# Optimization experiments

Hardware: AMD Instinct MI355X
Metric: run time of the kernel (lower is better)

The kernel has to match this reference:

```python
import jax, jax.numpy as jnp
import numpy as np

T, J, IC = 243, 17, 32
C = J * IC            # 544 embed dim
BS = 3                # block_size
NB = T // BS          # 81 num_blocks
K = 6                 # top_k
H = 8                 # num_heads
DEPTH = 2
HID = int(C * 2.0)    # 1088 mlp hidden
EPS = 1e-6


def _ln(x, g, b):
    m = x.mean(-1, keepdims=True)
    v = ((x - m) ** 2).mean(-1, keepdims=True)
    return (x - m) * jax.lax.rsqrt(v + EPS) * g + b


def setup_inputs() -> dict:
    key = jax.random.key(0)
    ks = jax.random.split(key, 16)
    s = 0.02
    B = 512
    return {
        "x": jax.random.normal(ks[0], (B, T, J, IC), jnp.float32),
        "pos_embed": s * jax.random.normal(ks[1], (1, T, C), jnp.float32),
        "fc1_w": s * jax.random.normal(ks[2], (NB, NB), jnp.float32),
        "fc2_w": s * jax.random.normal(ks[3], (NB, NB), jnp.float32),
        "ln1_g": jnp.ones((DEPTH, C), jnp.float32),
        "ln1_b": jnp.zeros((DEPTH, C), jnp.float32),
        "qkv_w": s * jax.random.normal(ks[4], (DEPTH, 3 * C, C), jnp.float32),
        "qkv_b": jnp.zeros((DEPTH, 3 * C), jnp.float32),
        "proj_w": s * jax.random.normal(ks[5], (DEPTH, C, C), jnp.float32),
        "proj_b": jnp.zeros((DEPTH, C), jnp.float32),
        "ln2_g": jnp.ones((DEPTH, C), jnp.float32),
        "ln2_b": jnp.zeros((DEPTH, C), jnp.float32),
        "mfc1_w": s * jax.random.normal(ks[6], (DEPTH, HID, C), jnp.float32),
        "mfc1_b": jnp.zeros((DEPTH, HID), jnp.float32),
        "mfc2_w": s * jax.random.normal(ks[7], (DEPTH, C, HID), jnp.float32),
        "mfc2_b": jnp.zeros((DEPTH, C), jnp.float32),
        "lnf_g": jnp.ones((C,), jnp.float32),
        "lnf_b": jnp.zeros((C,), jnp.float32),
        "wm2_w": s * jax.random.normal(ks[8], (K,), jnp.float32),
        "wm2_b": jnp.zeros((1,), jnp.float32),
    }


def reference(x, pos_embed, fc1_w, fc2_w, ln1_g, ln1_b, qkv_w, qkv_b,
              proj_w, proj_b, ln2_g, ln2_b, mfc1_w, mfc1_b, mfc2_w, mfc2_b,
              lnf_g, lnf_b, wm2_w, wm2_b):
    B = x.shape[0]
    x = x.reshape(B, T, C) + pos_embed                       # [B,T,C]
    # time_shift: zero-pad one frame at the front, keep first T rows, first C/2 chans
    shifted = jnp.pad(x, ((0, 0), (1, 0), (0, 0)))[:, :T, :C // 2]
    x = jnp.concatenate([shifted, x[:, :, C // 2:]], axis=2)
    # block pooling
    xb = x.reshape(B, NB, BS, C).mean(axis=2)                # [B,NB,C]
    # BlockAttention: global avg over C -> gated MLP -> topk -> gather
    y = xb.mean(axis=2)                                      # [B,NB]
    y = jax.nn.sigmoid(jnp.maximum(y @ fc1_w.T, 0.0) @ fc2_w.T)
    _, idx = jax.lax.top_k(y, K)                             # [B,K]
    t = jnp.take_along_axis(xb, idx[:, :, None], axis=1)     # [B,K,C]
    scale = (C // H) ** -0.5
    for i in range(DEPTH):
        h = _ln(t, ln1_g[i], ln1_b[i])
        qkv = (h @ qkv_w[i].T + qkv_b[i]).reshape(B, K, 3, H, C // H)
        q, k, v = qkv[:, :, 0], qkv[:, :, 1], qkv[:, :, 2]   # [B,K,H,hd]
        attn = jax.nn.softmax(jnp.einsum('bnhd,bmhd->bhnm', q, k) * scale, axis=-1)
        o = jnp.einsum('bhnm,bmhd->bnhd', attn, v).reshape(B, K, C)
        t = t + o @ proj_w[i].T + proj_b[i]
        h = _ln(t, ln2_g[i], ln2_b[i])
        h = jax.nn.gelu(h @ mfc1_w[i].T + mfc1_b[i], approximate=False)
        t = t + (h @ mfc2_w[i].T + mfc2_b[i])
    t = _ln(t, lnf_g, lnf_b)
    out = jnp.einsum('bkc,k->bc', t, wm2_w) + wm2_b          # Conv1d(K,1,ks=1)
    return out.reshape(B, 1, J, C // J)
```

## Files before the change

### kernel.cpp

```cpp
#include <hip/hip_runtime.h>
#include <hip/hip_bf16.h>
#include <math.h>

#define TT 243
#define CC 544
#define NBB 81
#define KK 6
#define HH 8
#define HD 68
#define DEPTH 2
#define HID 1088
#define BB 512
#define MTOK 3072
#define EPSF 1e-6f

typedef __attribute__((ext_vector_type(8))) short bf16x8;
typedef __attribute__((ext_vector_type(4))) float f32x4;

__device__ __forceinline__ __hip_bfloat16 f2b(float f) { return __float2bfloat16(f); }
__device__ __forceinline__ unsigned short f2bu(float f) {
    __hip_bfloat16 h = __float2bfloat16(f);
    return *(unsigned short*)&h;
}
__device__ __forceinline__ float b2f_lo(unsigned int u) { return __uint_as_float(u << 16); }
__device__ __forceinline__ float b2f_hi(unsigned int u) { return __uint_as_float(u & 0xffff0000u); }

#define E0 443904
#define E1 591872
#define E2 887808
#define E3 1183744

#define RS_BLOCKS 3888
#define PS_BLOCKS 8
#define WC_BLOCKS 4624
#define BW_GRID (RS_BLOCKS + PS_BLOCKS + WC_BLOCKS)

__global__ __launch_bounds__(256, 4) void bw_kernel(
    const float* __restrict__ x,
    const float* __restrict__ pos,
    const float* __restrict__ qkvw, const float* __restrict__ projw,
    const float* __restrict__ mfc1w, const float* __restrict__ mfc2w,
    unsigned short* __restrict__ wbf,
    float* __restrict__ L,
    float* __restrict__ R,
    float* __restrict__ pLR)
{
    const int blk = blockIdx.x;
    const int tid = threadIdx.x;

    if (blk < RS_BLOCKS) {
        const int w = tid >> 6;
        const int lane = tid & 63;
        const int oct = lane & 7;
        const int rsub = lane >> 3;
        const int r = (blk * 4 + w) * 8 + rsub;
        const float4* xr = (const float4*)x + (size_t)r * 136;
        float4 xs[17];
#pragma unroll
        for (int j = 0; j < 17; ++j) xs[j] = xr[oct + j * 8];
        float aL = 0.0f, aR = 0.0f;
#pragma unroll
        for (int j = 0; j < 17; ++j) {
            const float s = (xs[j].x + xs[j].y) + (xs[j].z + xs[j].w);
            if (j < 8) aL += s;
            else if (j == 8) { if (oct < 4) aL += s; else aR += s; }
            else aR += s;
        }
#pragma unroll
        for (int m = 1; m < 8; m <<= 1) {
            aL += __shfl_xor(aL, m);
            aR += __shfl_xor(aR, m);
        }
        if (oct == 0) { L[r] = aL; R[r] = aR; }
        return;
    }

    if (blk < RS_BLOCKS + PS_BLOCKS) {
        const int w = tid >> 6;
        const int lane = tid & 63;
        const int oct = lane & 7;
        const int rsub = lane >> 3;
        const int r = (blk - RS_BLOCKS) * 32 + w * 8 + rsub;
        const int rc = (r < TT) ? r : (TT - 1);
        const float4* pr = (const float4*)pos + (size_t)rc * 136;
        float4 xs[17];
#pragma unroll
        for (int j = 0; j < 17; ++j) xs[j] = pr[oct + j * 8];
        float aL = 0.0f, aR = 0.0f;
#pragma unroll
        for (int j = 0; j < 17; ++j) {
            const float s = (xs[j].x + xs[j].y) + (xs[j].z + xs[j].w);
            if (j < 8) aL += s;
            else if (j == 8) { if (oct < 4) aL += s; else aR += s; }
            else aR += s;
        }
#pragma unroll
        for (int m = 1; m < 8; m <<= 1) {
            aL += __shfl_xor(aL, m);
            aR += __shfl_xor(aR, m);
        }
        if (oct == 0 && r < TT) { pLR[r] = aL; pLR[TT + r] = aR; }
        return;
    }

    const int i = (blk - RS_BLOCKS - PS_BLOCKS) * 256 + tid;
    if (i < E3) {
        float4 v;
        if (i < E0)      v = ((const float4*)qkvw)[i];
        else if (i < E1) v = ((const float4*)projw)[i - E0];
        else if (i < E2) v = ((const float4*)mfc1w)[i - E1];
        else             v = ((const float4*)mfc2w)[i - E2];
        ushort4 o;
        o.x = f2bu(v.x); o.y = f2bu(v.y); o.z = f2bu(v.z); o.w = f2bu(v.w);
        ((ushort4*)wbf)[i] = o;
    }
}

__global__ __launch_bounds__(128) void select_kernel(
    const float* __restrict__ L,
    const float* __restrict__ R,
    const float* __restrict__ pLR,
    const float* __restrict__ fc1,
    const float* __restrict__ fc2,
    const float* __restrict__ x,
    const float* __restrict__ pos,
    const float* __restrict__ ln1g,
    const float* __restrict__ ln1b,
    float* __restrict__ t,
    unsigned short* __restrict__ hb)
{
    const int b = blockIdx.x;
    const int tid = threadIdx.x;
    __shared__ float sy[NBB], sz[NBB], swv[NBB];
    __shared__ int sidx[KK];
    __shared__ __align__(16) float st[KK][CC];

    const int w = tid >> 6;
    const int lane = tid & 63;
    const float4* x4 = (const float4*)x;
    const float4* p4 = (const float4*)pos;

    if (tid < NBB) {
        const int n = tid;
        const float* Lb = L + (size_t)b * TT;
        const float* Rb = R + (size_t)b * TT;
        const float* pL = pLR;
        const float* pR = pLR + TT;
        float s = Lb[3 * n] + Lb[3 * n + 1] + Rb[3 * n] + Rb[3 * n + 1] + Rb[3 * n + 2]
                + pL[3 * n] + pL[3 * n + 1] + pR[3 * n] + pR[3 * n + 1] + pR[3 * n + 2];
        if (n > 0) s += Lb[3 * n - 1] + pL[3 * n - 1];
        sy[n] = s * (1.0f / (3.0f * (float)CC));
    }
    __syncthreads();
    if (tid < NBB) {
        float s = 0.0f;
        for (int j = 0; j < NBB; ++j) s += fc1[tid * NBB + j] * sy[j];
        sz[tid] = fmaxf(s, 0.0f);
    }
    __syncthreads();
    if (tid < NBB) {
        float s = 0.0f;
        for (int j = 0; j < NBB; ++j) s += fc2[tid * NBB + j] * sz[j];
        swv[tid] = 1.0f / (1.0f + expf(-s));
    }
    __syncthreads();
    if (w == 0) {
        float va = (lane < NBB) ? swv[lane] : -1e30f;
        float vb = (lane + 64 < NBB) ? swv[lane + 64] : -1e30f;
        const int ia = lane, ib = lane + 64;
        for (int kk = 0; kk < KK; ++kk) {
            float v = va; int idx = ia;
            if (vb > v) { v = vb; idx = ib; }
#pragma unroll
            for (int m = 1; m < 64; m <<= 1) {
                const float ov = __shfl_xor(v, m);
                const int oi = __shfl_xor(idx, m);
                if (ov > v || (ov == v && oi < idx)) { v = ov; idx = oi; }
            }
            if (lane == 0) sidx[kk] = idx;
            if (ia == idx) va = -1e30f;
            if (ib == idx) vb = -1e30f;
        }
    }
    __syncthreads();

    for (int i = tid; i < KK * 136; i += 128) {
        const int k = i / 136;
        const int c4 = i - k * 136;
        const int n = sidx[k];
        const int shift = (c4 < 68) ? -1 : 0;
        float ax = 0.f, ay = 0.f, az = 0.f, aw = 0.f;
#pragma unroll
        for (int i2 = 0; i2 < 3; ++i2) {
            const int ttr = 3 * n + i2 + shift;
            if (ttr >= 0) {
                const float4 xv = x4[((size_t)b * TT + ttr) * 136 + c4];
                const float4 pv = p4[(size_t)ttr * 136 + c4];
                ax += xv.x + pv.x; ay += xv.y + pv.y; az += xv.z + pv.z; aw += xv.w + pv.w;
            }
        }
        const float inv3 = 1.0f / 3.0f;
        const float4 a = make_float4(ax * inv3, ay * inv3, az * inv3, aw * inv3);
        *(float4*)&st[k][c4 * 4] = a;
        ((float4*)t)[((size_t)b * KK + k) * 136 + c4] = a;
    }
    __syncthreads();

    for (int k = w; k < KK; k += 2) {
        float s = 0.0f, s2 = 0.0f;
        for (int c = lane; c < CC; c += 64) { const float v = st[k][c]; s += v; s2 += v * v; }
#pragma unroll
        for (int off = 32; off; off >>= 1) {
            s += __shfl_xor(s, off);
            s2 += __shfl_xor(s2, off);
        }
        const float m = s / (float)CC;
        const float inv = rsqrtf(s2 / (float)CC - m * m + EPSF);
        for (int c4 = lane; c4 < 136; c4 += 64) {
            const float4 v = *(const float4*)&st[k][c4 * 4];
            const float4 gv = ((const float4*)ln1g)[c4];
            const float4 bv = ((const float4*)ln1b)[c4];
            ushort4 o;
            o.x = f2bu((v.x - m) * inv * gv.x + bv.x);
            o.y = f2bu((v.y - m) * inv * gv.y + bv.y);
            o.z = f2bu((v.z - m) * inv * gv.z + bv.z);
            o.w = f2bu((v.w - m) * inv * gv.w + bv.w);
            ((ushort4*)hb)[((size_t)b * KK + k) * 136 + c4] = o;
        }
    }
}

__global__ __launch_bounds__(256) void ln_bf16_kernel(
    const float* __restrict__ X,
    const float* __restrict__ g,
    const float* __restrict__ bta,
    unsigned short* __restrict__ Y)
{
    const int row = blockIdx.x * 4 + (threadIdx.x >> 6);
    const int lane = threadIdx.x & 63;
    const float4* xr4 = (const float4*)(X + (size_t)row * CC);
    const float4 v0 = xr4[lane];
    const float4 v1 = xr4[lane + 64];
    float4 v2 = make_float4(0.f, 0.f, 0.f, 0.f);
    if (lane < 8) v2 = xr4[lane + 128];
    float s = (v0.x + v0.y + v0.z + v0.w) + (v1.x + v1.y + v1.z + v1.w)
            + (v2.x + v2.y + v2.z + v2.w);
    float s2 = (v0.x * v0.x + v0.y * v0.y + v0.z * v0.z + v0.w * v0.w)
             + (v1.x * v1.x + v1.y * v1.y + v1.z * v1.z + v1.w * v1.w)
             + (v2.x * v2.x + v2.y * v2.y + v2.z * v2.z + v2.w * v2.w);
#pragma unroll
    for (int off = 32; off; off >>= 1) {
        s += __shfl_xor(s, off);
        s2 += __shfl_xor(s2, off);
    }
    const float m = s / (float)CC;
    const float inv = rsqrtf(s2 / (float)CC - m * m + EPSF);
    ushort4* yr = (ushort4*)(Y + (size_t)row * CC);
    {
        const float4 gv = ((const float4*)g)[lane];
        const float4 bv = ((const float4*)bta)[lane];
        ushort4 o;
        o.x = f2bu((v0.x - m) * inv * gv.x + bv.x);
        o.y = f2bu((v0.y - m) * inv * gv.y + bv.y);
        o.z = f2bu((v0.z - m) * inv * gv.z + bv.z);
        o.w = f2bu((v0.w - m) * inv * gv.w + bv.w);
        yr[lane] = o;
    }
    {
        const float4 gv = ((const float4*)g)[lane + 64];
        const float4 bv = ((const float4*)bta)[lane + 64];
        ushort4 o;
        o.x = f2bu((v1.x - m) * inv * gv.x + bv.x);
        o.y = f2bu((v1.y - m) * inv * gv.y + bv.y);
        o.z = f2bu((v1.z - m) * inv * gv.z + bv.z);
        o.w = f2bu((v1.w - m) * inv * gv.w + bv.w);
        yr[lane + 64] = o;
    }
    if (lane < 8) {
        const float4 gv = ((const float4*)g)[lane + 128];
        const float4 bv = ((const float4*)bta)[lane + 128];
        ushort4 o;
        o.x = f2bu((v2.x - m) * inv * gv.x + bv.x);
        o.y = f2bu((v2.y - m) * inv * gv.y + bv.y);
        o.z = f2bu((v2.z - m) * inv * gv.z + bv.z);
        o.w = f2bu((v2.w - m) * inv * gv.w + bv.w);
        yr[lane + 128] = o;
    }
}

template <int ACT, int RES, int OBF>
__global__ __launch_bounds__(256) void gemm_mfma_kernel(
    const unsigned short* __restrict__ X,
    const unsigned short* __restrict__ W,
    const float* __restrict__ bias,
    const float* __restrict__ R,
    void* __restrict__ Y,
    int M, int N, int Kd)
{
    const int bm = blockIdx.y * 128;
    const int bn = blockIdx.x * 128;
    const int tid = threadIdx.x;
    const int K8 = Kd >> 3;

    __shared__ __align__(16) short As[128][40];
    __shared__ __align__(16) short Bs[128][40];

    const int r0 = tid >> 2;
    const int c0 = tid & 3;
    const int r1 = r0 + 64;

    const uint4* Xu = (const uint4*)X;
    const uint4* Wu = (const uint4*)W;

    const int wid = tid >> 6;
    const int lane = tid & 63;
    const int wm = (wid >> 1) * 64;
    const int wn = (wid & 1) * 64;
    const int l16 = lane & 15;
    const int l4 = lane >> 4;
    const int koff = l4 * 8;

    f32x4 acc[4][4] = {};

    const int wr0 = min(bn + r0, N - 1);
    const int wr1 = min(bn + r1, N - 1);

    uint4 a0 = Xu[(size_t)(bm + r0) * K8 + c0];
    uint4 a1 = Xu[(size_t)(bm + r1) * K8 + c0];
    uint4 b0 = Wu[(size_t)wr0 * K8 + c0];
    uint4 b1 = Wu[(size_t)wr1 * K8 + c0];

    const int nk = Kd >> 5;
    for (int kt = 0; kt < nk; ++kt) {
        __syncthreads();
        *(uint4*)&As[r0][c0 * 8] = a0;
        *(uint4*)&As[r1][c0 * 8] = a1;
        *(uint4*)&Bs[r0][c0 * 8] = b0;
        *(uint4*)&Bs[r1][c0 * 8] = b1;
        __syncthreads();

        const bool more = (kt + 1 < nk);
        uint4 na0, na1, nb0, nb1;
        if (more) {
            const int kc = (kt + 1) * 4 + c0;
            na0 = Xu[(size_t)(bm + r0) * K8 + kc];
            na1 = Xu[(size_t)(bm + r1) * K8 + kc];
            nb0 = Wu[(size_t)wr0 * K8 + kc];
            nb1 = Wu[(size_t)wr1 * K8 + kc];
        }

        bf16x8 af[4], bf[4];
#pragma unroll
        for (int mf = 0; mf < 4; ++mf) af[mf] = *(const bf16x8*)&As[wm + mf * 16 + l16][koff];
#pragma unroll
        for (int nf = 0; nf < 4; ++nf) bf[nf] = *(const bf16x8*)&Bs[wn + nf * 16 + l16][koff];
#pragma unroll
        for (int mf = 0; mf < 4; ++mf)
#pragma unroll
            for (int nf = 0; nf < 4; ++nf)
                acc[mf][nf] = __builtin_amdgcn_mfma_f32_16x16x32_bf16(af[mf], bf[nf], acc[mf][nf], 0, 0, 0);

        if (more) { a0 = na0; a1 = na1; b0 = nb0; b1 = nb1; }
    }

#pragma unroll
    for (int nf = 0; nf < 4; ++nf) {
        const int col = bn + wn + nf * 16 + l16;
        if (col < N) {
            const float bs = bias[col];
#pragma unroll
            for (int mf = 0; mf < 4; ++mf) {
#pragma unroll
                for (int j = 0; j < 4; ++j) {
                    const int row = bm + wm + mf * 16 + l4 * 4 + j;
                    float v = acc[mf][nf][j] + bs;
                    if (ACT == 1) v = 0.5f * v * (1.0f + erff(v * 0.70710678118654752f));
                    if (RES) v += R[(size_t)row * N + col];
                    if (OBF) ((__hip_bfloat16*)Y)[(size_t)row * N + col] = f2b(v);
                    else     ((float*)Y)[(size_t)row * N + col] = v;
                }
            }
        }
    }
}

__global__ __launch_bounds__(512) void attn_kernel(
    const unsigned short* __restrict__ qkv,
    __hip_bfloat16* __restrict__ o)
{
    const int b = blockIdx.x;
    __shared__ __align__(16) float sq[KK * 3 * CC];
    __shared__ float sp[HH][40];
    const int tid = threadIdx.x;

    const uint4* src4 = (const uint4*)(qkv + (size_t)b * KK * 3 * CC);
    for (int i = tid; i < (KK * 3 * CC) / 8; i += 512) {
        const uint4 u = src4[i];
        float4 f0, f1;
        f0.x = b2f_lo(u.x); f0.y = b2f_hi(u.x);
        f0.z = b2f_lo(u.y); f0.w = b2f_hi(u.y);
        f1.x = b2f_lo(u.z); f1.y = b2f_hi(u.z);
        f1.z = b2f_lo(u.w); f1.w = b2f_hi(u.w);
        ((float4*)sq)[2 * i] = f0;
        ((float4*)sq)[2 * i + 1] = f1;
    }
    __syncthreads();

    const int h = tid >> 6;
    const int lane = tid & 63;
    const float scl = rsqrtf((float)HD);

    if (lane < KK * KK) {
        const int n = lane / KK, m = lane - (lane / KK) * KK;
        const float* qp = &sq[n * (3 * CC) + 0 * CC + h * HD];
        const float* kp = &sq[m * (3 * CC) + 1 * CC + h * HD];
        float s = 0.0f;
#pragma unroll 4
        for (int d = 0; d < HD; ++d) s += qp[d] * kp[d];
        sp[h][lane] = s * scl;
    }
    __syncthreads();
    if (lane < KK) {
        const int n = lane;
        float mx = -1e30f;
#pragma unroll
        for (int m = 0; m < KK; ++m) mx = fmaxf(mx, sp[h][n * KK + m]);
        float e[KK];
        float sum = 0.0f;
#pragma unroll
        for (int m = 0; m < KK; ++m) { e[m] = expf(sp[h][n * KK + m] - mx); sum += e[m]; }
        const float inv = 1.0f / sum;
#pragma unroll
        for (int m = 0; m < KK; ++m) sp[h][n * KK + m] = e[m] * inv;
    }
    __syncthreads();
    for (int i = tid; i < KK * CC; i += 512) {
        const int n = i / CC;
        const int cd = i - n * CC;
        const int hh = cd / HD;
        const int d = cd - hh * HD;
        float acc = 0.0f;
#pragma unroll
        for (int m = 0; m < KK; ++m)
            acc += sp[hh][n * KK + m] * sq[m * (3 * CC) + 2 * CC + hh * HD + d];
        o[(size_t)b * KK * CC + i] = f2b(acc);
    }
}

__global__ __launch_bounds__(256) void final_kernel(
    const float* __restrict__ t,
    const float* __restrict__ g,
    const float* __restrict__ bta,
    const float* __restrict__ wm2w,
    const float* __restrict__ wm2b,
    float* __restrict__ out)
{
    const int b = blockIdx.x;
    const int tid = threadIdx.x;
    __shared__ float st[KK][CC];
    __shared__ float sm[KK], si[KK];
    const float* tb = t + (size_t)b * KK * CC;
    for (int i = tid; i < KK * CC; i += 256) st[i / CC][i % CC] = tb[i];
    __syncthreads();
    const int wid = tid >> 6, lane = tid & 63;
    for (int r = wid; r < KK; r += 4) {
        float s = 0.0f, s2 = 0.0f;
        for (int c = lane; c < CC; c += 64) { const float v = st[r][c]; s += v; s2 += v * v; }
#pragma unroll
        for (int off = 32; off; off >>= 1) { s += __shfl_xor(s, off); s2 += __shfl_xor(s2, off); }
        if (lane == 0) {
            const float m = s / (float)CC;
            sm[r] = m;
            si[r] = rsqrtf(s2 / (float)CC - m * m + EPSF);
        }
    }
    __syncthreads();
    const float w0 = wm2w[0], w1 = wm2w[1], w2 = wm2w[2], w3 = wm2w[3], w4 = wm2w[4], w5 = wm2w[5];
    const float wb = wm2b[0];
    for (int c = tid; c < CC; c += 256) {
        const float gg = g[c], bb = bta[c];
        float acc = wb;
        acc += w0 * ((st[0][c] - sm[0]) * si[0] * gg + bb);
        acc += w1 * ((st[1][c] - sm[1]) * si[1] * gg + bb);
        acc += w2 * ((st[2][c] - sm[2]) * si[2] * gg + bb);
        acc += w3 * ((st[3][c] - sm[3]) * si[3] * gg + bb);
        acc += w4 * ((st[4][c] - sm[4]) * si[4] * gg + bb);
        acc += w5 * ((st[5][c] - sm[5]) * si[5] * gg + bb);
        out[(size_t)b * CC + c] = acc;
    }
}

extern "C" void kernel_launch(void* const* d_in, const int* in_sizes, int n_in,
                              void* d_out, int out_size, void* d_ws, size_t ws_size,
                              hipStream_t stream)
{
    const float* x      = (const float*)d_in[0];
    const float* pos    = (const float*)d_in[1];
    const float* fc1_w  = (const float*)d_in[2];
    const float* fc2_w  = (const float*)d_in[3];
    const float* ln1_g  = (const float*)d_in[4];
    const float* ln1_b  = (const float*)d_in[5];
    const float* qkv_w  = (const float*)d_in[6];
    const float* qkv_b  = (const float*)d_in[7];
    const float* proj_w = (const float*)d_in[8];
    const float* proj_b = (const float*)d_in[9];
    const float* ln2_g  = (const float*)d_in[10];
    const float* ln2_b  = (const float*)d_in[11];
    const float* mfc1_w = (const float*)d_in[12];
    const float* mfc1_b = (const float*)d_in[13];
    const float* mfc2_w = (const float*)d_in[14];
    const float* mfc2_b = (const float*)d_in[15];
    const float* lnf_g  = (const float*)d_in[16];
    const float* lnf_b  = (const float*)d_in[17];
    const float* wm2_w  = (const float*)d_in[18];
    const float* wm2_b  = (const float*)d_in[19];

    float* ws = (float*)d_ws;
    float* L    = ws;
    float* R    = L + 124416;
    float* pLR  = R + 124416;
    float* t    = pLR + 512;
    unsigned short* qkvb = (unsigned short*)(t + (size_t)MTOK * CC);
    unsigned short* hb  = qkvb + (size_t)MTOK * 3 * CC;
    unsigned short* ob  = hb + (size_t)MTOK * CC;
    unsigned short* gb  = ob + (size_t)MTOK * CC;
    unsigned short* wbf = gb + (size_t)MTOK * HID;

    unsigned short* wqkv = wbf;
    unsigned short* wprj = wbf + 1775616;
    unsigned short* wf1  = wbf + 2367488;
    unsigned short* wf2  = wbf + 3551232;

    bw_kernel<<<BW_GRID, 256, 0, stream>>>(
        x, pos, qkv_w, proj_w, mfc1_w, mfc2_w, wbf, L, R, pLR);

    select_kernel<<<BB, 128, 0, stream>>>(
        L, R, pLR, fc1_w, fc2_w, x, pos, ln1_g, ln1_b, t, hb);

    for (int i = 0; i < DEPTH; ++i) {
        if (i > 0) {
            ln_bf16_kernel<<<MTOK / 4, 256, 0, stream>>>(t, ln1_g + i * CC, ln1_b + i * CC, hb);
        }
        gemm_mfma_kernel<0, 0, 1><<<dim3(13, 24), 256, 0, stream>>>(
            hb, wqkv + (size_t)i * 1632 * 544, qkv_b + (size_t)i * 3 * CC,
            nullptr, qkvb, MTOK, 3 * CC, CC);
        attn_kernel<<<BB, 512, 0, stream>>>(qkvb, (__hip_bfloat16*)ob);
        gemm_mfma_kernel<0, 1, 0><<<dim3(5, 24), 256, 0, stream>>>(
            ob, wprj + (size_t)i * 544 * 544, proj_b + (size_t)i * CC,
            t, t, MTOK, CC, CC);
        ln_bf16_kernel<<<MTOK / 4, 256, 0, stream>>>(t, ln2_g + i * CC, ln2_b + i * CC, hb);
        gemm_mfma_kernel<1, 0, 1><<<dim3(9, 24), 256, 0, stream>>>(
            hb, wf1 + (size_t)i * HID * 544, mfc1_b + (size_t)i * HID,
            nullptr, gb, MTOK, HID, CC);
        gemm_mfma_kernel<0, 1, 0><<<dim3(5, 24), 256, 0, stream>>>(
            gb, wf2 + (size_t)i * 544 * HID, mfc2_b + (size_t)i * CC,
            t, t, MTOK, CC, HID);
    }

    final_kernel<<<BB, 256, 0, stream>>>(t, lnf_g, lnf_b, wm2_w, wm2_b, (float*)d_out);
}
```

Measured before the change: 272.7 us.

## Fuse LayerNorm into GEMM A-tile loading and drop standalone LN kernels

```diff
diff --git a/kernel.cpp b/kernel.cpp
--- a/kernel.cpp
+++ b/kernel.cpp
@@ -124,21 +124,24 @@
     const float* __restrict__ fc2,
     const float* __restrict__ x,
     const float* __restrict__ pos,
-    const float* __restrict__ ln1g,
-    const float* __restrict__ ln1b,
-    float* __restrict__ t,
-    unsigned short* __restrict__ hb)
+    float* __restrict__ t)
 {
     const int b = blockIdx.x;
     const int tid = threadIdx.x;
+    __shared__ float sf1[NBB * NBB];
+    __shared__ float sf2[NBB * NBB];
     __shared__ float sy[NBB], sz[NBB], swv[NBB];
     __shared__ int sidx[KK];
-    __shared__ __align__(16) float st[KK][CC];
 
     const int w = tid >> 6;
     const int lane = tid & 63;
     const float4* x4 = (const float4*)x;
     const float4* p4 = (const float4*)pos;
+
+    for (int i = tid; i < NBB * NBB; i += 128) {
+        sf1[i] = fc1[i];
+        sf2[i] = fc2[i];
+    }
 
     if (tid < NBB) {
         const int n = tid;
@@ -154,13 +157,13 @@
     __syncthreads();
     if (tid < NBB) {
         float s = 0.0f;
-        for (int j = 0; j < NBB; ++j) s += fc1[tid * NBB + j] * sy[j];
+        for (int j = 0; j < NBB; ++j) s += sf1[tid * NBB + j] * sy[j];
         sz[tid] = fmaxf(s, 0.0f);
     }
     __syncthreads();
     if (tid < NBB) {
         float s = 0.0f;
-        for (int j = 0; j < NBB; ++j) s += fc2[tid * NBB + j] * sz[j];
+        for (int j = 0; j < NBB; ++j) s += sf2[tid * NBB + j] * sz[j];
         swv[tid] = 1.0f / (1.0f + expf(-s));
     }
     __syncthreads();
@@ -200,100 +203,19 @@
             }
         }
         const float inv3 = 1.0f / 3.0f;
-        const float4 a = make_float4(ax * inv3, ay * inv3, az * inv3, aw * inv3);
-        *(float4*)&st[k][c4 * 4] = a;
-        ((float4*)t)[((size_t)b * KK + k) * 136 + c4] = a;
-    }
-    __syncthreads();
-
-    for (int k = w; k < KK; k += 2) {
-        float s = 0.0f, s2 = 0.0f;
-        for (int c = lane; c < CC; c += 64) { const float v = st[k][c]; s += v; s2 += v * v; }
-#pragma unroll
-        for (int off = 32; off; off >>= 1) {
-            s += __shfl_xor(s, off);
-            s2 += __shfl_xor(s2, off);
-        }
-        const float m = s / (float)CC;
-        const float inv = rsqrtf(s2 / (float)CC - m * m + EPSF);
-        for (int c4 = lane; c4 < 136; c4 += 64) {
-            const float4 v = *(const float4*)&st[k][c4 * 4];
-            const float4 gv = ((const float4*)ln1g)[c4];
-            const float4 bv = ((const float4*)ln1b)[c4];
-            ushort4 o;
-            o.x = f2bu((v.x - m) * inv * gv.x + bv.x);
-            o.y = f2bu((v.y - m) * inv * gv.y + bv.y);
-            o.z = f2bu((v.z - m) * inv * gv.z + bv.z);
-            o.w = f2bu((v.w - m) * inv * gv.w + bv.w);
-            ((ushort4*)hb)[((size_t)b * KK + k) * 136 + c4] = o;
-        }
-    }
-}
-
-__global__ __launch_bounds__(256) void ln_bf16_kernel(
-    const float* __restrict__ X,
-    const float* __restrict__ g,
-    const float* __restrict__ bta,
-    unsigned short* __restrict__ Y)
-{
-    const int row = blockIdx.x * 4 + (threadIdx.x >> 6);
-    const int lane = threadIdx.x & 63;
-    const float4* xr4 = (const float4*)(X + (size_t)row * CC);
-    const float4 v0 = xr4[lane];
-    const float4 v1 = xr4[lane + 64];
-    float4 v2 = make_float4(0.f, 0.f, 0.f, 0.f);
-    if (lane < 8) v2 = xr4[lane + 128];
-    float s = (v0.x + v0.y + v0.z + v0.w) + (v1.x + v1.y + v1.z + v1.w)
-            + (v2.x + v2.y + v2.z + v2.w);
-    float s2 = (v0.x * v0.x + v0.y * v0.y + v0.z * v0.z + v0.w * v0.w)
-             + (v1.x * v1.x + v1.y * v1.y + v1.z * v1.z + v1.w * v1.w)
-             + (v2.x * v2.x + v2.y * v2.y + v2.z * v2.z + v2.w * v2.w);
-#pragma unroll
-    for (int off = 32; off; off >>= 1) {
-        s += __shfl_xor(s, off);
-        s2 += __shfl_xor(s2, off);
-    }
-    const float m = s / (float)CC;
-    const float inv = rsqrtf(s2 / (float)CC - m * m + EPSF);
-    ushort4* yr = (ushort4*)(Y + (size_t)row * CC);
-    {
-        const float4 gv = ((const float4*)g)[lane];
-        const float4 bv = ((const float4*)bta)[lane];
-        ushort4 o;
-        o.x = f2bu((v0.x - m) * inv * gv.x + bv.x);
-        o.y = f2bu((v0.y - m) * inv * gv.y + bv.y);
-        o.z = f2bu((v0.z - m) * inv * gv.z + bv.z);
-        o.w = f2bu((v0.w - m) * inv * gv.w + bv.w);
-        yr[lane] = o;
-    }
-    {
-        const float4 gv = ((const float4*)g)[lane + 64];
-        const float4 bv = ((const float4*)bta)[lane + 64];
-        ushort4 o;
-        o.x = f2bu((v1.x - m) * inv * gv.x + bv.x);
-        o.y = f2bu((v1.y - m) * inv * gv.y + bv.y);
-        o.z = f2bu((v1.z - m) * inv * gv.z + bv.z);
-        o.w = f2bu((v1.w - m) * inv * gv.w + bv.w);
-        yr[lane + 64] = o;
-    }
-    if (lane < 8) {
-        const float4 gv = ((const float4*)g)[lane + 128];
-        const float4 bv = ((const float4*)bta)[lane + 128];
-        ushort4 o;
-        o.x = f2bu((v2.x - m) * inv * gv.x + bv.x);
-        o.y = f2bu((v2.y - m) * inv * gv.y + bv.y);
-        o.z = f2bu((v2.z - m) * inv * gv.z + bv.z);
-        o.w = f2bu((v2.w - m) * inv * gv.w + bv.w);
-        yr[lane + 128] = o;
-    }
-}
-
-template <int ACT, int RES, int OBF>
+        ((float4*)t)[((size_t)b * KK + k) * 136 + c4] =
+            make_float4(ax * inv3, ay * inv3, az * inv3, aw * inv3);
+    }
+}
+
+template <int LNA, int ACT, int RES, int OBF>
 __global__ __launch_bounds__(256) void gemm_mfma_kernel(
-    const unsigned short* __restrict__ X,
+    const void* __restrict__ Xv,
     const unsigned short* __restrict__ W,
     const float* __restrict__ bias,
-    const float* __restrict__ R,
+    const float* __restrict__ Rr,
+    const float* __restrict__ lng,
+    const float* __restrict__ lnb,
     void* __restrict__ Y,
     int M, int N, int Kd)
 {
@@ -301,17 +223,18 @@
     const int bn = blockIdx.x * 128;
     const int tid = threadIdx.x;
     const int K8 = Kd >> 3;
+    const int K4 = Kd >> 2;
 
     __shared__ __align__(16) short As[128][40];
     __shared__ __align__(16) short Bs[128][40];
+    __shared__ float smean[LNA ? 128 : 1];
+    __shared__ float sinv[LNA ? 128 : 1];
+    __shared__ float sg[LNA ? CC : 1];
+    __shared__ float sb[LNA ? CC : 1];
 
     const int r0 = tid >> 2;
     const int c0 = tid & 3;
     const int r1 = r0 + 64;
-
-    const uint4* Xu = (const uint4*)X;
-    const uint4* Wu = (const uint4*)W;
-
     const int wid = tid >> 6;
     const int lane = tid & 63;
     const int wm = (wid >> 1) * 64;
@@ -320,33 +243,117 @@
     const int l4 = lane >> 4;
     const int koff = l4 * 8;
 
+    if constexpr (LNA) {
+        for (int i = tid; i < 136; i += 256) {
+            ((float4*)sg)[i] = ((const float4*)lng)[i];
+            ((float4*)sb)[i] = ((const float4*)lnb)[i];
+        }
+        const float4* Xf = (const float4*)Xv;
+        const int oct = lane & 7;
+        const int rsub = lane >> 3;
+#pragma unroll
+        for (int p = 0; p < 4; ++p) {
+            const int row = p * 32 + wid * 8 + rsub;
+            const float4* tr = Xf + (size_t)(bm + row) * 136;
+            float4 xs[17];
+#pragma unroll
+            for (int j = 0; j < 17; ++j) xs[j] = tr[oct + j * 8];
+            float s = 0.f, s2 = 0.f;
+#pragma unroll
+            for (int j = 0; j < 17; ++j) {
+                s += (xs[j].x + xs[j].y) + (xs[j].z + xs[j].w);
+                s2 += xs[j].x * xs[j].x + xs[j].y * xs[j].y
+                    + xs[j].z * xs[j].z + xs[j].w * xs[j].w;
+            }
+#pragma unroll
+            for (int m = 1; m < 8; m <<= 1) {
+                s += __shfl_xor(s, m);
+                s2 += __shfl_xor(s2, m);
+            }
+            if (oct == 0) {
+                const float mm = s / (float)CC;
+                smean[row] = mm;
+                sinv[row] = rsqrtf(s2 / (float)CC - mm * mm + EPSF);
+            }
+        }
+        __syncthreads();
+    }
+
     f32x4 acc[4][4] = {};
 
+    const uint4* Wu = (const uint4*)W;
     const int wr0 = min(bn + r0, N - 1);
     const int wr1 = min(bn + r1, N - 1);
 
-    uint4 a0 = Xu[(size_t)(bm + r0) * K8 + c0];
-    uint4 a1 = Xu[(size_t)(bm + r1) * K8 + c0];
+    uint4 a0, a1;
+    float4 f00, f01, f10, f11;
+    if constexpr (LNA) {
+        const float4* Xf = (const float4*)Xv;
+        const size_t base0 = (size_t)(bm + r0) * K4 + c0 * 2;
+        const size_t base1 = (size_t)(bm + r1) * K4 + c0 * 2;
+        f00 = Xf[base0]; f01 = Xf[base0 + 1];
+        f10 = Xf[base1]; f11 = Xf[base1 + 1];
+    } else {
+        const uint4* Xu = (const uint4*)Xv;
+        a0 = Xu[(size_t)(bm + r0) * K8 + c0];
+        a1 = Xu[(size_t)(bm + r1) * K8 + c0];
+    }
     uint4 b0 = Wu[(size_t)wr0 * K8 + c0];
     uint4 b1 = Wu[(size_t)wr1 * K8 + c0];
 
     const int nk = Kd >> 5;
     for (int kt = 0; kt < nk; ++kt) {
         __syncthreads();
-        *(uint4*)&As[r0][c0 * 8] = a0;
-        *(uint4*)&As[r1][c0 * 8] = a1;
+        if constexpr (LNA) {
+            const int cb = kt * 32 + c0 * 8;
+            const float m0 = smean[r0], i0 = sinv[r0];
+            const float m1 = smean[r1], i1 = sinv[r1];
+            ushort4 o;
+            o.x = f2bu((f00.x - m0) * i0 * sg[cb + 0] + sb[cb + 0]);
+            o.y = f2bu((f00.y - m0) * i0 * sg[cb + 1] + sb[cb + 1]);
+            o.z = f2bu((f00.z - m0) * i0 * sg[cb + 2] + sb[cb + 2]);
+            o.w = f2bu((f00.w - m0) * i0 * sg[cb + 3] + sb[cb + 3]);
+            *(ushort4*)&As[r0][c0 * 8] = o;
+            o.x = f2bu((f01.x - m0) * i0 * sg[cb + 4] + sb[cb + 4]);
+            o.y = f2bu((f01.y - m0) * i0 * sg[cb + 5] + sb[cb + 5]);
+            o.z = f2bu((f01.z - m0) * i0 * sg[cb + 6] + sb[cb + 6]);
+            o.w = f2bu((f01.w - m0) * i0 * sg[cb + 7] + sb[cb + 7]);
+            *(ushort4*)&As[r0][c0 * 8 + 4] = o;
+            o.x = f2bu((f10.x - m1) * i1 * sg[cb + 0] + sb[cb + 0]);
+            o.y = f2bu((f10.y - m1) * i1 * sg[cb + 1] + sb[cb + 1]);
+            o.z = f2bu((f10.z - m1) * i1 * sg[cb + 2] + sb[cb + 2]);
+            o.w = f2bu((f10.w - m1) * i1 * sg[cb + 3] + sb[cb + 3]);
+            *(ushort4*)&As[r1][c0 * 8] = o;
+            o.x = f2bu((f11.x - m1) * i1 * sg[cb + 4] + sb[cb + 4]);
+            o.y = f2bu((f11.y - m1) * i1 * sg[cb + 5] + sb[cb + 5]);
+            o.z = f2bu((f11.z - m1) * i1 * sg[cb + 6] + sb[cb + 6]);
+            o.w = f2bu((f11.w - m1) * i1 * sg[cb + 7] + sb[cb + 7]);
+            *(ushort4*)&As[r1][c0 * 8 + 4] = o;
+        } else {
+            *(uint4*)&As[r0][c0 * 8] = a0;
+            *(uint4*)&As[r1][c0 * 8] = a1;
+        }
         *(uint4*)&Bs[r0][c0 * 8] = b0;
         *(uint4*)&Bs[r1][c0 * 8] = b1;
         __syncthreads();
 
         const bool more = (kt + 1 < nk);
-        uint4 na0, na1, nb0, nb1;
         if (more) {
+            if constexpr (LNA) {
+                const float4* Xf = (const float4*)Xv;
+                const size_t base0 = (size_t)(bm + r0) * K4 + (kt + 1) * 8 + c0 * 2;
+                const size_t base1 = (size_t)(bm + r1) * K4 + (kt + 1) * 8 + c0 * 2;
+                f00 = Xf[base0]; f01 = Xf[base0 + 1];
+                f10 = Xf[base1]; f11 = Xf[base1 + 1];
+            } else {
+                const uint4* Xu = (const uint4*)Xv;
+                const int kc = (kt + 1) * 4 + c0;
+                a0 = Xu[(size_t)(bm + r0) * K8 + kc];
+                a1 = Xu[(size_t)(bm + r1) * K8 + kc];
+            }
             const int kc = (kt + 1) * 4 + c0;
-            na0 = Xu[(size_t)(bm + r0) * K8 + kc];
-            na1 = Xu[(size_t)(bm + r1) * K8 + kc];
-            nb0 = Wu[(size_t)wr0 * K8 + kc];
-            nb1 = Wu[(size_t)wr1 * K8 + kc];
+            b0 = Wu[(size_t)wr0 * K8 + kc];
+            b1 = Wu[(size_t)wr1 * K8 + kc];
         }
 
         bf16x8 af[4], bf[4];
@@ -359,8 +366,6 @@
 #pragma unroll
             for (int nf = 0; nf < 4; ++nf)
                 acc[mf][nf] = __builtin_amdgcn_mfma_f32_16x16x32_bf16(af[mf], bf[nf], acc[mf][nf], 0, 0, 0);
-
-        if (more) { a0 = na0; a1 = na1; b0 = nb0; b1 = nb1; }
     }
 
 #pragma unroll
@@ -375,7 +380,7 @@
                     const int row = bm + wm + mf * 16 + l4 * 4 + j;
                     float v = acc[mf][nf][j] + bs;
                     if (ACT == 1) v = 0.5f * v * (1.0f + erff(v * 0.70710678118654752f));
-                    if (RES) v += R[(size_t)row * N + col];
+                    if (RES) v += Rr[(size_t)row * N + col];
                     if (OBF) ((__hip_bfloat16*)Y)[(size_t)row * N + col] = f2b(v);
                     else     ((float*)Y)[(size_t)row * N + col] = v;
                 }
@@ -521,8 +526,7 @@
     float* pLR  = R + 124416;
     float* t    = pLR + 512;
     unsigned short* qkvb = (unsigned short*)(t + (size_t)MTOK * CC);
-    unsigned short* hb  = qkvb + (size_t)MTOK * 3 * CC;
-    unsigned short* ob  = hb + (size_t)MTOK * CC;
+    unsigned short* ob  = qkvb + (size_t)MTOK * 3 * CC;
     unsigned short* gb  = ob + (size_t)MTOK * CC;
     unsigned short* wbf = gb + (size_t)MTOK * HID;
 
@@ -535,26 +539,22 @@
         x, pos, qkv_w, proj_w, mfc1_w, mfc2_w, wbf, L, R, pLR);
 
     select_kernel<<<BB, 128, 0, stream>>>(
-        L, R, pLR, fc1_w, fc2_w, x, pos, ln1_g, ln1_b, t, hb);
+        L, R, pLR, fc1_w, fc2_w, x, pos, t);
 
     for (int i = 0; i < DEPTH; ++i) {
-        if (i > 0) {
-            ln_bf16_kernel<<<MTOK / 4, 256, 0, stream>>>(t, ln1_g + i * CC, ln1_b + i * CC, hb);
-        }
-        gemm_mfma_kernel<0, 0, 1><<<dim3(13, 24), 256, 0, stream>>>(
-            hb, wqkv + (size_t)i * 1632 * 544, qkv_b + (size_t)i * 3 * CC,
-            nullptr, qkvb, MTOK, 3 * CC, CC);
+        gemm_mfma_kernel<1, 0, 0, 1><<<dim3(13, 24), 256, 0, stream>>>(
+            t, wqkv + (size_t)i * 1632 * 544, qkv_b + (size_t)i * 3 * CC,
+            nullptr, ln1_g + i * CC, ln1_b + i * CC, qkvb, MTOK, 3 * CC, CC);
         attn_kernel<<<BB, 512, 0, stream>>>(qkvb, (__hip_bfloat16*)ob);
-        gemm_mfma_kernel<0, 1, 0><<<dim3(5, 24), 256, 0, stream>>>(
+        gemm_mfma_kernel<0, 0, 1, 0><<<dim3(5, 24), 256, 0, stream>>>(
             ob, wprj + (size_t)i * 544 * 544, proj_b + (size_t)i * CC,
-            t, t, MTOK, CC, CC);
-        ln_bf16_kernel<<<MTOK / 4, 256, 0, stream>>>(t, ln2_g + i * CC, ln2_b + i * CC, hb);
-        gemm_mfma_kernel<1, 0, 1><<<dim3(9, 24), 256, 0, stream>>>(
-            hb, wf1 + (size_t)i * HID * 544, mfc1_b + (size_t)i * HID,
-            nullptr, gb, MTOK, HID, CC);
-        gemm_mfma_kernel<0, 1, 0><<<dim3(5, 24), 256, 0, stream>>>(
+            t, nullptr, nullptr, t, MTOK, CC, CC);
+        gemm_mfma_kernel<1, 1, 0, 1><<<dim3(9, 24), 256, 0, stream>>>(
+            t, wf1 + (size_t)i * HID * 544, mfc1_b + (size_t)i * HID,
+            nullptr, ln2_g + i * CC, ln2_b + i * CC, gb, MTOK, HID, CC);
+        gemm_mfma_kernel<0, 0, 1, 0><<<dim3(5, 24), 256, 0, stream>>>(
             gb, wf2 + (size_t)i * 544 * HID, mfc2_b + (size_t)i * CC,
-            t, t, MTOK, CC, HID);
+            t, nullptr, nullptr, t, MTOK, CC, HID);
     }
 
     final_kernel<<<BB, 256, 0, stream>>>(t, lnf_g, lnf_b, wm2_w, wm2_b, (float*)d_out);
```

Result: slower. 287.4 us (+5.4%).

## Double GEMM K-tile to 64 and stage fc weights in LDS for selection

Applied to the files above, without the earlier changes.

```diff
diff --git a/kernel.cpp b/kernel.cpp
--- a/kernel.cpp
+++ b/kernel.cpp
@@ -117,20 +117,18 @@
 }
 
 __global__ __launch_bounds__(128) void select_kernel(
-    const float* __restrict__ L,
-    const float* __restrict__ R,
+    const float* __restrict__ L, const float* __restrict__ R,
     const float* __restrict__ pLR,
-    const float* __restrict__ fc1,
-    const float* __restrict__ fc2,
-    const float* __restrict__ x,
-    const float* __restrict__ pos,
-    const float* __restrict__ ln1g,
-    const float* __restrict__ ln1b,
+    const float* __restrict__ fc1, const float* __restrict__ fc2,
+    const float* __restrict__ x, const float* __restrict__ pos,
+    const float* __restrict__ ln1g, const float* __restrict__ ln1b,
     float* __restrict__ t,
     unsigned short* __restrict__ hb)
 {
     const int b = blockIdx.x;
     const int tid = threadIdx.x;
+    __shared__ float sf1[NBB * NBB];
+    __shared__ float sf2[NBB * NBB];
     __shared__ float sy[NBB], sz[NBB], swv[NBB];
     __shared__ int sidx[KK];
     __shared__ __align__(16) float st[KK][CC];
@@ -139,6 +137,11 @@
     const int lane = tid & 63;
     const float4* x4 = (const float4*)x;
     const float4* p4 = (const float4*)pos;
+
+    for (int i = tid; i < NBB * NBB; i += 128) {
+        sf1[i] = fc1[i];
+        sf2[i] = fc2[i];
+    }
 
     if (tid < NBB) {
         const int n = tid;
@@ -154,13 +157,13 @@
     __syncthreads();
     if (tid < NBB) {
         float s = 0.0f;
-        for (int j = 0; j < NBB; ++j) s += fc1[tid * NBB + j] * sy[j];
+        for (int j = 0; j < NBB; ++j) s += sf1[tid * NBB + j] * sy[j];
         sz[tid] = fmaxf(s, 0.0f);
     }
     __syncthreads();
     if (tid < NBB) {
         float s = 0.0f;
-        for (int j = 0; j < NBB; ++j) s += fc2[tid * NBB + j] * sz[j];
+        for (int j = 0; j < NBB; ++j) s += sf2[tid * NBB + j] * sz[j];
         swv[tid] = 1.0f / (1.0f + expf(-s));
     }
     __syncthreads();
@@ -231,10 +234,8 @@
 }
 
 __global__ __launch_bounds__(256) void ln_bf16_kernel(
-    const float* __restrict__ X,
-    const float* __restrict__ g,
-    const float* __restrict__ bta,
-    unsigned short* __restrict__ Y)
+    const float* __restrict__ X, const float* __restrict__ g,
+    const float* __restrict__ bta, unsigned short* __restrict__ Y)
 {
     const int row = blockIdx.x * 4 + (threadIdx.x >> 6);
     const int lane = threadIdx.x & 63;
@@ -293,7 +294,7 @@
     const unsigned short* __restrict__ X,
     const unsigned short* __restrict__ W,
     const float* __restrict__ bias,
-    const float* __restrict__ R,
+    const float* __restrict__ Rr,
     void* __restrict__ Y,
     int M, int N, int Kd)
 {
@@ -302,8 +303,8 @@
     const int tid = threadIdx.x;
     const int K8 = Kd >> 3;
 
-    __shared__ __align__(16) short As[128][40];
-    __shared__ __align__(16) short Bs[128][40];
+    __shared__ __align__(16) short As[128][72];
+    __shared__ __align__(16) short Bs[128][72];
 
     const int r0 = tid >> 2;
     const int c0 = tid & 3;
@@ -325,42 +326,61 @@
     const int wr0 = min(bn + r0, N - 1);
     const int wr1 = min(bn + r1, N - 1);
 
-    uint4 a0 = Xu[(size_t)(bm + r0) * K8 + c0];
-    uint4 a1 = Xu[(size_t)(bm + r1) * K8 + c0];
-    uint4 b0 = Wu[(size_t)wr0 * K8 + c0];
-    uint4 b1 = Wu[(size_t)wr1 * K8 + c0];
-
-    const int nk = Kd >> 5;
+    const uint4 zz = {0u, 0u, 0u, 0u};
+    uint4 a00, a01, a10, a11, b00, b01, b10, b11;
+    {
+        const int k1 = c0, k2 = c0 + 4;
+        a00 = (k1 < K8) ? Xu[(size_t)(bm + r0) * K8 + k1] : zz;
+        a01 = (k2 < K8) ? Xu[(size_t)(bm + r0) * K8 + k2] : zz;
+        a10 = (k1 < K8) ? Xu[(size_t)(bm + r1) * K8 + k1] : zz;
+        a11 = (k2 < K8) ? Xu[(size_t)(bm + r1) * K8 + k2] : zz;
+        b00 = (k1 < K8) ? Wu[(size_t)wr0 * K8 + k1] : zz;
+        b01 = (k2 < K8) ? Wu[(size_t)wr0 * K8 + k2] : zz;
+        b10 = (k1 < K8) ? Wu[(size_t)wr1 * K8 + k1] : zz;
+        b11 = (k2 < K8) ? Wu[(size_t)wr1 * K8 + k2] : zz;
+    }
+
+    const int nk = (Kd + 63) >> 6;
     for (int kt = 0; kt < nk; ++kt) {
         __syncthreads();
-        *(uint4*)&As[r0][c0 * 8] = a0;
-        *(uint4*)&As[r1][c0 * 8] = a1;
-        *(uint4*)&Bs[r0][c0 * 8] = b0;
-        *(uint4*)&Bs[r1][c0 * 8] = b1;
+        *(uint4*)&As[r0][c0 * 8]       = a00;
+        *(uint4*)&As[r0][(c0 + 4) * 8] = a01;
+        *(uint4*)&As[r1][c0 * 8]       = a10;
+        *(uint4*)&As[r1][(c0 + 4) * 8] = a11;
+        *(uint4*)&Bs[r0][c0 * 8]       = b00;
+        *(uint4*)&Bs[r0][(c0 + 4) * 8] = b01;
+        *(uint4*)&Bs[r1][c0 * 8]       = b10;
+        *(uint4*)&Bs[r1][(c0 + 4) * 8] = b11;
         __syncthreads();
 
-        const bool more = (kt + 1 < nk);
-        uint4 na0, na1, nb0, nb1;
-        if (more) {
-            const int kc = (kt + 1) * 4 + c0;
-            na0 = Xu[(size_t)(bm + r0) * K8 + kc];
-            na1 = Xu[(size_t)(bm + r1) * K8 + kc];
-            nb0 = Wu[(size_t)wr0 * K8 + kc];
-            nb1 = Wu[(size_t)wr1 * K8 + kc];
-        }
-
-        bf16x8 af[4], bf[4];
-#pragma unroll
-        for (int mf = 0; mf < 4; ++mf) af[mf] = *(const bf16x8*)&As[wm + mf * 16 + l16][koff];
-#pragma unroll
-        for (int nf = 0; nf < 4; ++nf) bf[nf] = *(const bf16x8*)&Bs[wn + nf * 16 + l16][koff];
-#pragma unroll
-        for (int mf = 0; mf < 4; ++mf)
+        if (kt + 1 < nk) {
+            const int k1 = (kt + 1) * 8 + c0;
+            const int k2 = k1 + 4;
+            a00 = (k1 < K8) ? Xu[(size_t)(bm + r0) * K8 + k1] : zz;
+            a01 = (k2 < K8) ? Xu[(size_t)(bm + r0) * K8 + k2] : zz;
+            a10 = (k1 < K8) ? Xu[(size_t)(bm + r1) * K8 + k1] : zz;
+            a11 = (k2 < K8) ? Xu[(size_t)(bm + r1) * K8 + k2] : zz;
+            b00 = (k1 < K8) ? Wu[(size_t)wr0 * K8 + k1] : zz;
+            b01 = (k2 < K8) ? Wu[(size_t)wr0 * K8 + k2] : zz;
+            b10 = (k1 < K8) ? Wu[(size_t)wr1 * K8 + k1] : zz;
+            b11 = (k2 < K8) ? Wu[(size_t)wr1 * K8 + k2] : zz;
+        }
+
+#pragma unroll
+        for (int kh = 0; kh < 2; ++kh) {
+            bf16x8 af[4], bf[4];
+#pragma unroll
+            for (int mf = 0; mf < 4; ++mf)
+                af[mf] = *(const bf16x8*)&As[wm + mf * 16 + l16][kh * 32 + koff];
 #pragma unroll
             for (int nf = 0; nf < 4; ++nf)
-                acc[mf][nf] = __builtin_amdgcn_mfma_f32_16x16x32_bf16(af[mf], bf[nf], acc[mf][nf], 0, 0, 0);
-
-        if (more) { a0 = na0; a1 = na1; b0 = nb0; b1 = nb1; }
+                bf[nf] = *(const bf16x8*)&Bs[wn + nf * 16 + l16][kh * 32 + koff];
+#pragma unroll
+            for (int mf = 0; mf < 4; ++mf)
+#pragma unroll
+                for (int nf = 0; nf < 4; ++nf)
+                    acc[mf][nf] = __builtin_amdgcn_mfma_f32_16x16x32_bf16(af[mf], bf[nf], acc[mf][nf], 0, 0, 0);
+        }
     }
 
 #pragma unroll
@@ -375,8 +395,8 @@
                     const int row = bm + wm + mf * 16 + l4 * 4 + j;
                     float v = acc[mf][nf][j] + bs;
                     if (ACT == 1) v = 0.5f * v * (1.0f + erff(v * 0.70710678118654752f));
-                    if (RES) v += R[(size_t)row * N + col];
-                    if (OBF) ((__hip_bfloat16*)Y)[(size_t)row * N + col] = f2b(v);
+                    if (RES) v += Rr[(size_t)row * N + col];
+                    if (OBF) ((unsigned short*)Y)[(size_t)row * N + col] = f2bu(v);
                     else     ((float*)Y)[(size_t)row * N + col] = v;
                 }
             }
@@ -448,12 +468,9 @@
 }
 
 __global__ __launch_bounds__(256) void final_kernel(
-    const float* __restrict__ t,
-    const float* __restrict__ g,
-    const float* __restrict__ bta,
-    const float* __restrict__ wm2w,
-    const float* __restrict__ wm2b,
-    float* __restrict__ out)
+    const float* __restrict__ t, const float* __restrict__ g,
+    const float* __restrict__ bta, const float* __restrict__ wm2w,
+    const float* __restrict__ wm2b, float* __restrict__ out)
 {
     const int b = blockIdx.x;
     const int tid = threadIdx.x;
```

After: 253.2 us. -7.1%, faster.
